# Kernel tuning notes

Hardware: AMD Instinct MI355X
Metric: run time of the kernel (lower is better)

Reference implementation:

```python
import jax, jax.numpy as jnp
import numpy as np

B, K, DIM, T_FRAMES = 4, 200, 256, 800

def _conv1d_same(x, w, b):
    # x: [B, K, Cin], w: [3, Cin, Cout] (WIO), 'same' padding over token axis
    y = jax.lax.conv_general_dilated(x, w, window_strides=(1,), padding='SAME',
                                     dimension_numbers=('NWC', 'WIO', 'NWC'))
    return y + b

def _swish_block(x, w1, b1, w2, b2):
    x = jax.nn.silu(x @ w1 + b1)
    return jax.nn.silu(x @ w2 + b2)

def setup_inputs() -> dict:
    key = jax.random.key(0)
    ks = jax.random.split(key, 10)
    def lin(k, fan_in, shape):
        return jax.random.normal(k, shape, dtype=jnp.float32) / np.sqrt(fan_in)
    inp = {
        'T': T_FRAMES,
        'durations': jax.random.uniform(ks[0], (B, K), dtype=jnp.float32) * 4.0,
        'features': jax.random.normal(ks[1], (B, K, DIM), dtype=jnp.float32),
        'conv1_w': lin(ks[2], 3 * DIM, (3, DIM, 8)),
        'conv1_b': jnp.zeros((8,), jnp.float32),
        'conv2_w': lin(ks[3], 3 * DIM, (3, DIM, 8)),
        'conv2_b': jnp.zeros((8,), jnp.float32),
        'sw1_w1': lin(ks[4], 10, (10, 16)), 'sw1_b1': jnp.zeros((16,), jnp.float32),
        'sw1_w2': lin(ks[5], 16, (16, 16)), 'sw1_b2': jnp.zeros((16,), jnp.float32),
        'sw2_w1': lin(ks[6], 10, (10, 2)), 'sw2_b1': jnp.zeros((2,), jnp.float32),
        'sw2_w2': lin(ks[7], 2, (2, 2)), 'sw2_b2': jnp.zeros((2,), jnp.float32),
        'p1_w': lin(ks[8], 2, (2, 1)), 'p1_b': jnp.zeros((1,), jnp.float32),
        'p2_w': lin(ks[9], 16, (16, DIM)), 'p2_b': jnp.zeros((DIM,), jnp.float32),
    }
    return inp

def reference(T, durations, features, conv1_w, conv1_b, conv2_w, conv2_b,
              sw1_w1, sw1_b1, sw1_w2, sw1_b2, sw2_w1, sw2_b1, sw2_w2, sw2_b2,
              p1_w, p1_b, p2_w, p2_b):
    # Conv + SiLU token feature extraction: [B, K, 8]
    left = jax.nn.silu(_conv1d_same(features, conv1_w, conv1_b))
    right = jax.nn.silu(_conv1d_same(features, conv2_w, conv2_b))
    # Token boundary grids S, E: [B, T, K]
    token_end = jnp.cumsum(durations, axis=1)          # [B, K]
    token_start = token_end - durations                # [B, K]
    t = jnp.arange(T, dtype=features.dtype)            # frame index grid
    S = t[None, :, None] - token_start[:, None, :]     # [B, T, K]
    E = token_end[:, None, :] - t[None, :, None]       # [B, T, K]
    Bn, Tn, Kn = S.shape
    # Concat (S, E, conv_feats) -> [B, T, K, 10]
    xleft = jnp.concatenate([S[..., None], E[..., None],
                             jnp.broadcast_to(left[:, None], (Bn, Tn, Kn, 8))], axis=-1)
    xright = jnp.concatenate([S[..., None], E[..., None],
                              jnp.broadcast_to(right[:, None], (Bn, Tn, Kn, 8))], axis=-1)
    C = _swish_block(xleft, sw1_w1, sw1_b1, sw1_w2, sw1_b2)      # [B, T, K, 16]
    r = _swish_block(xright, sw2_w1, sw2_b1, sw2_w2, sw2_b2)     # [B, T, K, 2]
    logits = (r @ p1_w + p1_b)[..., 0]                           # [B, T, K]
    W = jax.nn.softmax(logits, axis=-1)                          # attention over tokens
    # Upsampled output: weighted token features + projected auxiliary context
    O = jnp.einsum('btk,bkd->btd', W, features)
    A = jnp.einsum('btk,btkp->btp', W, C)                        # [B, T, 16]
    return O + (A @ p2_w + p2_b)
```

## Files before the change

### kernel.cpp

```cpp
#include <hip/hip_runtime.h>
#include <math.h>

#define B_   4
#define K_   200
#define DIM_ 256
#define T_   800

#define S_UP 68

__device__ __forceinline__ float silu_f(float x) {
    return x / (1.0f + __expf(-x));
}

__global__ __launch_bounds__(256) void prep_kernel(
        const float* __restrict__ dur,
        const float* __restrict__ feats,
        const float* __restrict__ c1w, const float* __restrict__ c1b,
        const float* __restrict__ c2w, const float* __restrict__ c2b,
        const float* __restrict__ sw1_w1, const float* __restrict__ sw1_b1,
        const float* __restrict__ sw2_w1, const float* __restrict__ sw2_b1,
        float* __restrict__ cw) {
    const int b = blockIdx.y, k0 = blockIdx.x * 16;
    const int tid = threadIdx.x, w = tid >> 6, l = tid & 63;

    __shared__ float wT[16][769];
    __shared__ float sSc[K_], sEc[K_];
    __shared__ float sfeat[16][16];

    for (int i = tid; i < 3 * DIM_ * 8; i += 256) {
        int tc = i >> 3, o = i & 7;
        wT[o][tc] = c1w[i];
    }
    for (int i = tid; i < 3 * DIM_ * 8; i += 256) {
        int tc = i >> 3, o = i & 7;
        wT[8 + o][tc] = c2w[i];
    }
    if (tid < 64) {
        float4 dv = make_float4(0.f, 0.f, 0.f, 0.f);
        if (tid < 50) dv = *(const float4*)&dur[b * K_ + tid * 4];
        float s0 = dv.x, s1 = s0 + dv.y, s2 = s1 + dv.z, s3 = s2 + dv.w;
        float sc = s3;
#pragma unroll
        for (int off = 1; off < 64; off <<= 1) {
            float v = __shfl_up(sc, off);
            if (tid >= off) sc += v;
        }
        float excl = sc - s3;
        if (tid < 50) {
            *(float4*)&sSc[tid * 4] = make_float4(excl, excl + s0, excl + s1, excl + s2);
            *(float4*)&sEc[tid * 4] = make_float4(excl + s0, excl + s1, excl + s2, excl + s3);
        }
    }
    __syncthreads();

    const int kl = w * 4 + (l >> 4);
    const int k  = k0 + kl;
    const int oc = l & 15, o = oc & 7;
    const float4* f4 = (const float4*)feats;
    float acc = 0.f;
#pragma unroll
    for (int tap = 0; tap < 3; ++tap) {
        int kk = k + tap - 1;
        bool valid = (kk >= 0 && kk < K_);
        int kc = valid ? kk : 0;
        const float4* fr = f4 + (size_t)(b * K_ + kc) * 64;
        float tacc = 0.f;
#pragma unroll 8
        for (int c4 = 0; c4 < 64; ++c4) {
            float4 fv = fr[c4];
            float4 wv = *(const float4*)&wT[oc][tap * DIM_ + c4 * 4];
            tacc += fv.x * wv.x + fv.y * wv.y + fv.z * wv.z + fv.w * wv.w;
        }
        acc += valid ? tacc : 0.f;
    }
    float bias = (oc < 8) ? c1b[o] : c2b[o];
    sfeat[kl][oc] = silu_f(acc + bias);
    __syncthreads();

    {
        const int j = tid >> 4, klc = tid & 15;
        const int kk = k0 + klc;
        if (kk < K_) {
            float st = sSc[kk], en = sEc[kk];
            float a = sw1_b1[j] - st * sw1_w1[j] + en * sw1_w1[16 + j];
#pragma unroll
            for (int i = 0; i < 8; ++i) a += sfeat[klc][i] * sw1_w1[(2 + i) * 16 + j];
            cw[(b * 18 + 2 + j) * K_ + kk] = a;
        }
    }
    if (tid < 32) {
        const int which = tid >> 4, klc = tid & 15;
        const int kk = k0 + klc;
        if (kk < K_) {
            float st = sSc[kk], en = sEc[kk];
            float a = sw2_b1[which] - st * sw2_w1[which] + en * sw2_w1[2 + which];
#pragma unroll
            for (int i = 0; i < 8; ++i) a += sfeat[klc][8 + i] * sw2_w1[(2 + i) * 2 + which];
            cw[(b * 18 + which) * K_ + kk] = a;
        }
    }
}

__global__ __launch_bounds__(256) void main_kernel(
        const float* __restrict__ feats,
        const float* __restrict__ cw,
        const float* __restrict__ sw1_w1, const float* __restrict__ sw1_w2,
        const float* __restrict__ sw1_b2,
        const float* __restrict__ sw2_w1, const float* __restrict__ sw2_w2,
        const float* __restrict__ sw2_b2,
        const float* __restrict__ p1_w,   const float* __restrict__ p1_b,
        const float* __restrict__ p2_w,   const float* __restrict__ p2_b,
        float* __restrict__ out) {
    const int t0 = blockIdx.x * 4, b = blockIdx.y;
    const int tid = threadIdx.x, w = tid >> 6, l = tid & 63;
    const int t = t0 + w;

    __shared__ alignas(16) float cb[18 * K_];
    __shared__ alignas(16) float upool[64 * S_UP];
    __shared__ alignas(16) float W4[K_][4];
    __shared__ alignas(16) float At[16][4];
    __shared__ float lw2T[16][16];
    __shared__ float lb2s[16];

    {
        const float4* cg4 = (const float4*)(cw + b * 18 * K_);
        float4* cb4 = (float4*)cb;
        for (int i = tid; i < 18 * K_ / 4; i += 256) cb4[i] = cg4[i];
    }
    lw2T[tid & 15][tid >> 4] = sw1_w2[tid];
    if (tid < 16) lb2s[tid] = sw1_b2[tid];
    __syncthreads();

    const float tf = (float)t;
    const float a0 = sw2_w1[0] - sw2_w1[2], a1 = sw2_w1[1] - sw2_w1[3];
    const float rw20 = sw2_w2[0], rw21 = sw2_w2[1], rw22 = sw2_w2[2], rw23 = sw2_w2[3];
    const float rb20 = sw2_b2[0], rb21 = sw2_b2[1];
    const float p10 = p1_w[0], p11 = p1_w[1], p1b0 = p1_b[0];

    float lg[4];
#pragma unroll
    for (int i = 0; i < 4; ++i) {
        int k = l + 64 * i;
        int kc = (k < K_) ? k : (K_ - 1);
        float h0 = silu_f(fmaf(a0, tf, cb[0 * K_ + kc]));
        float h1 = silu_f(fmaf(a1, tf, cb[1 * K_ + kc]));
        float g0 = silu_f(rb20 + h0 * rw20 + h1 * rw22);
        float g1 = silu_f(rb21 + h0 * rw21 + h1 * rw23);
        lg[i] = (k < K_) ? (g0 * p10 + g1 * p11 + p1b0) : -1e30f;
    }
    float m = fmaxf(fmaxf(lg[0], lg[1]), fmaxf(lg[2], lg[3]));
#pragma unroll
    for (int off = 32; off > 0; off >>= 1) m = fmaxf(m, __shfl_xor(m, off));
    float e0 = __expf(lg[0] - m), e1 = __expf(lg[1] - m);
    float e2 = __expf(lg[2] - m), e3 = __expf(lg[3] - m);
    float ssum = e0 + e1 + e2 + e3;
#pragma unroll
    for (int off = 32; off > 0; off >>= 1) ssum += __shfl_xor(ssum, off);
    float inv = 1.0f / ssum;
    float wgt[4] = { e0 * inv, e1 * inv, e2 * inv, e3 * inv };
#pragma unroll
    for (int i = 0; i < 4; ++i) { int k = l + 64 * i; if (k < K_) W4[k][w] = wgt[i]; }

    float ajt[16];
#pragma unroll
    for (int j = 0; j < 16; ++j) ajt[j] = (sw1_w1[j] - sw1_w1[16 + j]) * tf;

    float hmat[4][16];
#pragma unroll
    for (int j = 0; j < 16; ++j) {
#pragma unroll
        for (int i = 0; i < 4; ++i) {
            int k = l + 64 * i;
            int kc = (k < K_) ? k : (K_ - 1);
            hmat[i][j] = silu_f(ajt[j] + cb[(2 + j) * K_ + kc]);
        }
    }
    float acc[16];
#pragma unroll
    for (int j = 0; j < 16; ++j) {
        float4 w0 = *(const float4*)&lw2T[j][0];
        float4 w1v = *(const float4*)&lw2T[j][4];
        float4 w2v = *(const float4*)&lw2T[j][8];
        float4 w3v = *(const float4*)&lw2T[j][12];
        float bj = lb2s[j];
        float s = 0.f;
#pragma unroll
        for (int i = 0; i < 4; ++i) {
            float c = bj
                + hmat[i][0]  * w0.x  + hmat[i][1]  * w0.y  + hmat[i][2]  * w0.z  + hmat[i][3]  * w0.w
                + hmat[i][4]  * w1v.x + hmat[i][5]  * w1v.y + hmat[i][6]  * w1v.z + hmat[i][7]  * w1v.w
                + hmat[i][8]  * w2v.x + hmat[i][9]  * w2v.y + hmat[i][10] * w2v.z + hmat[i][11] * w2v.w
                + hmat[i][12] * w3v.x + hmat[i][13] * w3v.y + hmat[i][14] * w3v.z + hmat[i][15] * w3v.w;
            s += wgt[i] * silu_f(c);
        }
        acc[j] = s;
    }

#pragma unroll
    for (int j = 0; j < 16; ++j) upool[(w * 16 + j) * S_UP + l] = acc[j];
    __syncthreads();
    {
        int rwv = tid >> 6, rj = (tid >> 2) & 15, rq = tid & 3;
        const float* base = &upool[(rwv * 16 + rj) * S_UP + rq * 16];
        float4 b0 = *(const float4*)&base[0];
        float4 b1 = *(const float4*)&base[4];
        float4 b2 = *(const float4*)&base[8];
        float4 b3 = *(const float4*)&base[12];
        float s = b0.x + b0.y + b0.z + b0.w + b1.x + b1.y + b1.z + b1.w
                + b2.x + b2.y + b2.z + b2.w + b3.x + b3.y + b3.z + b3.w;
        s += __shfl_down(s, 1);
        s += __shfl_down(s, 2);
        if (rq == 0) At[rj][rwv] = s;
    }
    __syncthreads();

    {
        const float4* fB4 = (const float4*)(feats + (size_t)b * K_ * DIM_);
        float4 po[4];
#pragma unroll
        for (int f = 0; f < 4; ++f) po[f] = make_float4(0.f, 0.f, 0.f, 0.f);
        const int kb = w * 50;
        for (int kk = 0; kk < 50; ++kk) {
            int k = kb + kk;
            float4 wv = *(const float4*)&W4[k][0];
            float4 fv = fB4[k * 64 + l];
            po[0].x += wv.x * fv.x; po[0].y += wv.x * fv.y; po[0].z += wv.x * fv.z; po[0].w += wv.x * fv.w;
            po[1].x += wv.y * fv.x; po[1].y += wv.y * fv.y; po[1].z += wv.y * fv.z; po[1].w += wv.y * fv.w;
            po[2].x += wv.z * fv.x; po[2].y += wv.z * fv.y; po[2].z += wv.z * fv.z; po[2].w += wv.z * fv.w;
            po[3].x += wv.w * fv.x; po[3].y += wv.w * fv.y; po[3].z += wv.w * fv.z; po[3].w += wv.w * fv.w;
        }
#pragma unroll
        for (int f = 0; f < 4; ++f) {
            upool[(w * 16 + f * 4 + 0) * S_UP + l] = po[f].x;
            upool[(w * 16 + f * 4 + 1) * S_UP + l] = po[f].y;
            upool[(w * 16 + f * 4 + 2) * S_UP + l] = po[f].z;
            upool[(w * 16 + f * 4 + 3) * S_UP + l] = po[f].w;
        }
    }
    __syncthreads();

    {
        const int d = tid, l0 = d >> 2, q = d & 3;
        float v0 = 0.f, v1 = 0.f, v2 = 0.f, v3 = 0.f;
#pragma unroll
        for (int ww = 0; ww < 4; ++ww) {
            v0 += upool[(ww * 16 + 0 * 4 + q) * S_UP + l0];
            v1 += upool[(ww * 16 + 1 * 4 + q) * S_UP + l0];
            v2 += upool[(ww * 16 + 2 * 4 + q) * S_UP + l0];
            v3 += upool[(ww * 16 + 3 * 4 + q) * S_UP + l0];
        }
        float ab = p2_b[d];
        v0 += ab; v1 += ab; v2 += ab; v3 += ab;
#pragma unroll
        for (int p = 0; p < 16; ++p) {
            float pw = p2_w[p * DIM_ + d];
            float4 av = *(const float4*)&At[p][0];
            v0 += av.x * pw; v1 += av.y * pw; v2 += av.z * pw; v3 += av.w * pw;
        }
        float* op = out + ((size_t)b * T_ + t0) * DIM_ + d;
        op[0 * DIM_] = v0;
        op[1 * DIM_] = v1;
        op[2 * DIM_] = v2;
        op[3 * DIM_] = v3;
    }
}

extern "C" void kernel_launch(void* const* d_in, const int* in_sizes, int n_in,
                              void* d_out, int out_size, void* d_ws, size_t ws_size,
                              hipStream_t stream) {
    const float* durations = (const float*)d_in[1];
    const float* features  = (const float*)d_in[2];
    const float* conv1_w   = (const float*)d_in[3];
    const float* conv1_b   = (const float*)d_in[4];
    const float* conv2_w   = (const float*)d_in[5];
    const float* conv2_b   = (const float*)d_in[6];
    const float* sw1_w1    = (const float*)d_in[7];
    const float* sw1_b1    = (const float*)d_in[8];
    const float* sw1_w2    = (const float*)d_in[9];
    const float* sw1_b2    = (const float*)d_in[10];
    const float* sw2_w1    = (const float*)d_in[11];
    const float* sw2_b1    = (const float*)d_in[12];
    const float* sw2_w2    = (const float*)d_in[13];
    const float* sw2_b2    = (const float*)d_in[14];
    const float* p1_w      = (const float*)d_in[15];
    const float* p1_b      = (const float*)d_in[16];
    const float* p2_w      = (const float*)d_in[17];
    const float* p2_b      = (const float*)d_in[18];
    float* out = (float*)d_out;

    float* cw = (float*)d_ws;

    prep_kernel<<<dim3(13, B_), 256, 0, stream>>>(
        durations, features, conv1_w, conv1_b, conv2_w, conv2_b,
        sw1_w1, sw1_b1, sw2_w1, sw2_b1, cw);
    main_kernel<<<dim3(T_ / 4, B_), 256, 0, stream>>>(
        features, cw,
        sw1_w1, sw1_w2, sw1_b2,
        sw2_w1, sw2_w2, sw2_b2,
        p1_w, p1_b, p2_w, p2_b, out);
}
```

Before: 140.2 us.

## Split conv across channel lanes in prep, register-load token coefs and prefetch features in main

The prep kernel now handles 4 tokens per block over 50 blocks instead of 16 over 13. Each lane computes a partial conv dot product over its channel slice, and the partials are reduced through shared memory, replacing the serial per-thread 768-long loop. The main kernel drops the shared-memory staging of the coefficient table and loads the needed values straight into registers. It also prefetches the first 8 feature rows before the MLP work, gives the second reduction its own shared region so one barrier can be removed, and adds an occupancy hint of 3 blocks. The risks are higher register pressure and extra per-thread global loads in exchange for better parallelism and latency hiding.

```diff
diff --git a/kernel.cpp b/kernel.cpp
--- a/kernel.cpp
+++ b/kernel.cpp
@@ -20,19 +20,17 @@
         const float* __restrict__ sw1_w1, const float* __restrict__ sw1_b1,
         const float* __restrict__ sw2_w1, const float* __restrict__ sw2_b1,
         float* __restrict__ cw) {
-    const int b = blockIdx.y, k0 = blockIdx.x * 16;
+    const int b = blockIdx.y, k0 = blockIdx.x * 4;
     const int tid = threadIdx.x, w = tid >> 6, l = tid & 63;
 
-    __shared__ float wT[16][769];
+    __shared__ float wT[16][772];
+    __shared__ float red[64][S_UP];
     __shared__ float sSc[K_], sEc[K_];
-    __shared__ float sfeat[16][16];
+    __shared__ float sfeat[4][16];
 
     for (int i = tid; i < 3 * DIM_ * 8; i += 256) {
         int tc = i >> 3, o = i & 7;
-        wT[o][tc] = c1w[i];
-    }
-    for (int i = tid; i < 3 * DIM_ * 8; i += 256) {
-        int tc = i >> 3, o = i & 7;
+        wT[o][tc]     = c1w[i];
         wT[8 + o][tc] = c2w[i];
     }
     if (tid < 64) {
@@ -53,55 +51,70 @@
     }
     __syncthreads();
 
-    const int kl = w * 4 + (l >> 4);
-    const int k  = k0 + kl;
-    const int oc = l & 15, o = oc & 7;
-    const float4* f4 = (const float4*)feats;
-    float acc = 0.f;
-#pragma unroll
-    for (int tap = 0; tap < 3; ++tap) {
-        int kk = k + tap - 1;
-        bool valid = (kk >= 0 && kk < K_);
-        int kc = valid ? kk : 0;
-        const float4* fr = f4 + (size_t)(b * K_ + kc) * 64;
-        float tacc = 0.f;
-#pragma unroll 8
-        for (int c4 = 0; c4 < 64; ++c4) {
-            float4 fv = fr[c4];
-            float4 wv = *(const float4*)&wT[oc][tap * DIM_ + c4 * 4];
-            tacc += fv.x * wv.x + fv.y * wv.y + fv.z * wv.z + fv.w * wv.w;
-        }
-        acc += valid ? tacc : 0.f;
-    }
-    float bias = (oc < 8) ? c1b[o] : c2b[o];
-    sfeat[kl][oc] = silu_f(acc + bias);
-    __syncthreads();
-
-    {
-        const int j = tid >> 4, klc = tid & 15;
-        const int kk = k0 + klc;
-        if (kk < K_) {
-            float st = sSc[kk], en = sEc[kk];
-            float a = sw1_b1[j] - st * sw1_w1[j] + en * sw1_w1[16 + j];
-#pragma unroll
-            for (int i = 0; i < 8; ++i) a += sfeat[klc][i] * sw1_w1[(2 + i) * 16 + j];
-            cw[(b * 18 + 2 + j) * K_ + kk] = a;
-        }
-    }
-    if (tid < 32) {
-        const int which = tid >> 4, klc = tid & 15;
-        const int kk = k0 + klc;
-        if (kk < K_) {
-            float st = sSc[kk], en = sEc[kk];
-            float a = sw2_b1[which] - st * sw2_w1[which] + en * sw2_w1[2 + which];
-#pragma unroll
-            for (int i = 0; i < 8; ++i) a += sfeat[klc][8 + i] * sw2_w1[(2 + i) * 2 + which];
-            cw[(b * 18 + which) * K_ + kk] = a;
-        }
+    {
+        const int k = k0 + w;
+        const float4* f4 = (const float4*)feats;
+        float4 fv[3];
+#pragma unroll
+        for (int tap = 0; tap < 3; ++tap) {
+            int kk = k - 1 + tap;
+            bool valid = (kk >= 0 && kk < K_);
+            int kc = valid ? kk : 0;
+            float4 v = f4[(size_t)(b * K_ + kc) * 64 + l];
+            fv[tap] = valid ? v : make_float4(0.f, 0.f, 0.f, 0.f);
+        }
+        float acc[16];
+#pragma unroll
+        for (int oc = 0; oc < 16; ++oc) acc[oc] = 0.f;
+#pragma unroll
+        for (int tap = 0; tap < 3; ++tap) {
+#pragma unroll
+            for (int oc = 0; oc < 16; ++oc) {
+                float4 wv = *(const float4*)&wT[oc][tap * DIM_ + 4 * l];
+                acc[oc] += fv[tap].x * wv.x + fv[tap].y * wv.y
+                         + fv[tap].z * wv.z + fv[tap].w * wv.w;
+            }
+        }
+#pragma unroll
+        for (int oc = 0; oc < 16; ++oc) red[w * 16 + oc][l] = acc[oc];
+    }
+    __syncthreads();
+    {
+        const int rwv = tid >> 6, oc = (tid >> 2) & 15, rq = tid & 3;
+        const float* base = &red[rwv * 16 + oc][rq * 16];
+        float4 b0 = *(const float4*)&base[0];
+        float4 b1 = *(const float4*)&base[4];
+        float4 b2 = *(const float4*)&base[8];
+        float4 b3 = *(const float4*)&base[12];
+        float s = b0.x + b0.y + b0.z + b0.w + b1.x + b1.y + b1.z + b1.w
+                + b2.x + b2.y + b2.z + b2.w + b3.x + b3.y + b3.z + b3.w;
+        s += __shfl_down(s, 1);
+        s += __shfl_down(s, 2);
+        if (rq == 0) {
+            float bias = (oc < 8) ? c1b[oc] : c2b[oc & 7];
+            sfeat[rwv][oc] = silu_f(s + bias);
+        }
+    }
+    __syncthreads();
+
+    if (tid < 64) {
+        const int j = tid >> 2, klc = tid & 3, kk = k0 + klc;
+        float st = sSc[kk], en = sEc[kk];
+        float a = sw1_b1[j] - st * sw1_w1[j] + en * sw1_w1[16 + j];
+#pragma unroll
+        for (int i = 0; i < 8; ++i) a += sfeat[klc][i] * sw1_w1[(2 + i) * 16 + j];
+        cw[(b * 18 + 2 + j) * K_ + kk] = a;
+    } else if (tid < 72) {
+        const int idx = tid - 64, which = idx >> 2, klc = idx & 3, kk = k0 + klc;
+        float st = sSc[kk], en = sEc[kk];
+        float a = sw2_b1[which] - st * sw2_w1[which] + en * sw2_w1[2 + which];
+#pragma unroll
+        for (int i = 0; i < 8; ++i) a += sfeat[klc][8 + i] * sw2_w1[(2 + i) * 2 + which];
+        cw[(b * 18 + which) * K_ + kk] = a;
     }
 }
 
-__global__ __launch_bounds__(256) void main_kernel(
+__global__ __launch_bounds__(256, 3) void main_kernel(
         const float* __restrict__ feats,
         const float* __restrict__ cw,
         const float* __restrict__ sw1_w1, const float* __restrict__ sw1_w2,
@@ -115,20 +128,28 @@
     const int tid = threadIdx.x, w = tid >> 6, l = tid & 63;
     const int t = t0 + w;
 
-    __shared__ alignas(16) float cb[18 * K_];
-    __shared__ alignas(16) float upool[64 * S_UP];
+    __shared__ alignas(16) float upool[128 * S_UP];
     __shared__ alignas(16) float W4[K_][4];
     __shared__ alignas(16) float At[16][4];
     __shared__ float lw2T[16][16];
     __shared__ float lb2s[16];
 
-    {
-        const float4* cg4 = (const float4*)(cw + b * 18 * K_);
-        float4* cb4 = (float4*)cb;
-        for (int i = tid; i < 18 * K_ / 4; i += 256) cb4[i] = cg4[i];
-    }
     lw2T[tid & 15][tid >> 4] = sw1_w2[tid];
     if (tid < 16) lb2s[tid] = sw1_b2[tid];
+
+    const float* cbg = cw + b * 18 * K_;
+    int kc[4];
+#pragma unroll
+    for (int i = 0; i < 4; ++i) { int k = l + 64 * i; kc[i] = (k < K_) ? k : (K_ - 1); }
+    float Bv[4][16];
+#pragma unroll
+    for (int j = 0; j < 16; ++j)
+#pragma unroll
+        for (int i = 0; i < 4; ++i) Bv[i][j] = cbg[(2 + j) * K_ + kc[i]];
+    float c0[4], c1[4];
+#pragma unroll
+    for (int i = 0; i < 4; ++i) { c0[i] = cbg[kc[i]]; c1[i] = cbg[K_ + kc[i]]; }
+
     __syncthreads();
 
     const float tf = (float)t;
@@ -140,13 +161,11 @@
     float lg[4];
 #pragma unroll
     for (int i = 0; i < 4; ++i) {
-        int k = l + 64 * i;
-        int kc = (k < K_) ? k : (K_ - 1);
-        float h0 = silu_f(fmaf(a0, tf, cb[0 * K_ + kc]));
-        float h1 = silu_f(fmaf(a1, tf, cb[1 * K_ + kc]));
+        float h0 = silu_f(fmaf(a0, tf, c0[i]));
+        float h1 = silu_f(fmaf(a1, tf, c1[i]));
         float g0 = silu_f(rb20 + h0 * rw20 + h1 * rw22);
         float g1 = silu_f(rb21 + h0 * rw21 + h1 * rw23);
-        lg[i] = (k < K_) ? (g0 * p10 + g1 * p11 + p1b0) : -1e30f;
+        lg[i] = (l + 64 * i < K_) ? (g0 * p10 + g1 * p11 + p1b0) : -1e30f;
     }
     float m = fmaxf(fmaxf(lg[0], lg[1]), fmaxf(lg[2], lg[3]));
 #pragma unroll
@@ -161,20 +180,20 @@
 #pragma unroll
     for (int i = 0; i < 4; ++i) { int k = l + 64 * i; if (k < K_) W4[k][w] = wgt[i]; }
 
+    const int kb = w * 50;
+    const float4* fB4 = (const float4*)(feats + (size_t)b * K_ * DIM_);
+    float4 pf[8];
+#pragma unroll
+    for (int q = 0; q < 8; ++q) pf[q] = fB4[(size_t)(kb + q) * 64 + l];
+
     float ajt[16];
 #pragma unroll
     for (int j = 0; j < 16; ++j) ajt[j] = (sw1_w1[j] - sw1_w1[16 + j]) * tf;
-
     float hmat[4][16];
 #pragma unroll
-    for (int j = 0; j < 16; ++j) {
-#pragma unroll
-        for (int i = 0; i < 4; ++i) {
-            int k = l + 64 * i;
-            int kc = (k < K_) ? k : (K_ - 1);
-            hmat[i][j] = silu_f(ajt[j] + cb[(2 + j) * K_ + kc]);
-        }
-    }
+    for (int j = 0; j < 16; ++j)
+#pragma unroll
+        for (int i = 0; i < 4; ++i) hmat[i][j] = silu_f(ajt[j] + Bv[i][j]);
     float acc[16];
 #pragma unroll
     for (int j = 0; j < 16; ++j) {
@@ -195,12 +214,13 @@
         }
         acc[j] = s;
     }
-
 #pragma unroll
     for (int j = 0; j < 16; ++j) upool[(w * 16 + j) * S_UP + l] = acc[j];
-    __syncthreads();
-    {
-        int rwv = tid >> 6, rj = (tid >> 2) & 15, rq = tid & 3;
+
+    __syncthreads();
+
+    {
+        const int rwv = tid >> 6, rj = (tid >> 2) & 15, rq = tid & 3;
         const float* base = &upool[(rwv * 16 + rj) * S_UP + rq * 16];
         float4 b0 = *(const float4*)&base[0];
         float4 b1 = *(const float4*)&base[4];
@@ -212,29 +232,35 @@
         s += __shfl_down(s, 2);
         if (rq == 0) At[rj][rwv] = s;
     }
-    __syncthreads();
-
-    {
-        const float4* fB4 = (const float4*)(feats + (size_t)b * K_ * DIM_);
+
+    {
         float4 po[4];
 #pragma unroll
         for (int f = 0; f < 4; ++f) po[f] = make_float4(0.f, 0.f, 0.f, 0.f);
-        const int kb = w * 50;
-        for (int kk = 0; kk < 50; ++kk) {
-            int k = kb + kk;
-            float4 wv = *(const float4*)&W4[k][0];
-            float4 fv = fB4[k * 64 + l];
+#pragma unroll
+        for (int kk = 0; kk < 8; ++kk) {
+            float4 wv = *(const float4*)&W4[kb + kk][0];
+            float4 fv = pf[kk];
             po[0].x += wv.x * fv.x; po[0].y += wv.x * fv.y; po[0].z += wv.x * fv.z; po[0].w += wv.x * fv.w;
             po[1].x += wv.y * fv.x; po[1].y += wv.y * fv.y; po[1].z += wv.y * fv.z; po[1].w += wv.y * fv.w;
             po[2].x += wv.z * fv.x; po[2].y += wv.z * fv.y; po[2].z += wv.z * fv.z; po[2].w += wv.z * fv.w;
             po[3].x += wv.w * fv.x; po[3].y += wv.w * fv.y; po[3].z += wv.w * fv.z; po[3].w += wv.w * fv.w;
         }
+#pragma unroll 6
+        for (int kk = 8; kk < 50; ++kk) {
+            float4 wv = *(const float4*)&W4[kb + kk][0];
+            float4 fv = fB4[(size_t)(kb + kk) * 64 + l];
+            po[0].x += wv.x * fv.x; po[0].y += wv.x * fv.y; po[0].z += wv.x * fv.z; po[0].w += wv.x * fv.w;
+            po[1].x += wv.y * fv.x; po[1].y += wv.y * fv.y; po[1].z += wv.y * fv.z; po[1].w += wv.y * fv.w;
+            po[2].x += wv.z * fv.x; po[2].y += wv.z * fv.y; po[2].z += wv.z * fv.z; po[2].w += wv.z * fv.w;
+            po[3].x += wv.w * fv.x; po[3].y += wv.w * fv.y; po[3].z += wv.w * fv.z; po[3].w += wv.w * fv.w;
+        }
 #pragma unroll
         for (int f = 0; f < 4; ++f) {
-            upool[(w * 16 + f * 4 + 0) * S_UP + l] = po[f].x;
-            upool[(w * 16 + f * 4 + 1) * S_UP + l] = po[f].y;
-            upool[(w * 16 + f * 4 + 2) * S_UP + l] = po[f].z;
-            upool[(w * 16 + f * 4 + 3) * S_UP + l] = po[f].w;
+            upool[(64 + w * 16 + f * 4 + 0) * S_UP + l] = po[f].x;
+            upool[(64 + w * 16 + f * 4 + 1) * S_UP + l] = po[f].y;
+            upool[(64 + w * 16 + f * 4 + 2) * S_UP + l] = po[f].z;
+            upool[(64 + w * 16 + f * 4 + 3) * S_UP + l] = po[f].w;
         }
     }
     __syncthreads();
@@ -244,10 +270,10 @@
         float v0 = 0.f, v1 = 0.f, v2 = 0.f, v3 = 0.f;
 #pragma unroll
         for (int ww = 0; ww < 4; ++ww) {
-            v0 += upool[(ww * 16 + 0 * 4 + q) * S_UP + l0];
-            v1 += upool[(ww * 16 + 1 * 4 + q) * S_UP + l0];
-            v2 += upool[(ww * 16 + 2 * 4 + q) * S_UP + l0];
-            v3 += upool[(ww * 16 + 3 * 4 + q) * S_UP + l0];
+            v0 += upool[(64 + ww * 16 + 0 * 4 + q) * S_UP + l0];
+            v1 += upool[(64 + ww * 16 + 1 * 4 + q) * S_UP + l0];
+            v2 += upool[(64 + ww * 16 + 2 * 4 + q) * S_UP + l0];
+            v3 += upool[(64 + ww * 16 + 3 * 4 + q) * S_UP + l0];
         }
         float ab = p2_b[d];
         v0 += ab; v1 += ab; v2 += ab; v3 += ab;
@@ -290,7 +316,7 @@
 
     float* cw = (float*)d_ws;
 
-    prep_kernel<<<dim3(13, B_), 256, 0, stream>>>(
+    prep_kernel<<<dim3(50, B_), 256, 0, stream>>>(
         durations, features, conv1_w, conv1_b, conv2_w, conv2_b,
         sw1_w1, sw1_b1, sw2_w1, sw2_b1, cw);
     main_kernel<<<dim3(T_ / 4, B_), 256, 0, stream>>>(
```

After: 130.2 us. -7.1%, faster.
